# Kernel optimization log

Hardware: AMD Instinct MI355X
Metric: run time of the kernel (lower is better)

## Reference

```python
import math
import jax, jax.numpy as jnp
import numpy as np

N_HEADS = 16

def setup_inputs() -> dict:
    key = jax.random.key(0)
    k1, k2, k3 = jax.random.split(key, 3)
    B, S, D = 2, 2048, 1024
    x = jax.random.normal(k1, (B, S, D), dtype=jnp.float32)
    W_qkv = jax.random.normal(k2, (3 * D, D), dtype=jnp.float32)
    W_o = jax.random.normal(k3, (D, D), dtype=jnp.float32)
    return {"x": x, "W_qkv": W_qkv, "W_o": W_o}


def reference(x, W_qkv, W_o):
    B, S, D = x.shape
    H = N_HEADS
    d_h = D // H
    # fused QKV projection: (B,S,3D)
    t = jnp.matmul(x, W_qkv.T)
    t = t.reshape(B, S, 3, D)
    # NOTE: module reshapes (B,S,D) -> (B,H,S,d_h) directly (no transpose);
    # heads partition the flattened seq*feature layout. Replicate exactly.
    q = t[:, :, 0, :].reshape(B, H, S, d_h)
    k = t[:, :, 1, :].reshape(B, H, S, d_h)
    v = t[:, :, 2, :].reshape(B, H, S, d_h)
    # scaled by sqrt(d_model), as in the original (not sqrt(d_h))
    scores = jnp.einsum('bhqd,bhkd->bhqk', q, k) / math.sqrt(D)
    scores = jnp.tril(scores)
    # original sets ALL exact zeros to -inf (masks upper triangle)
    scores = jnp.where(scores == 0, -jnp.inf, scores)
    attn = jax.nn.softmax(scores, axis=-1)
    y_prime = jnp.matmul(attn, v)  # (B,H,S,d_h)
    y_prime = y_prime.transpose(0, 2, 1, 3).reshape(B, S, D)
    y = jnp.matmul(y_prime, W_o.T)
    return y
```

## Files before the change

### kernel.cpp

```cpp
#include <hip/hip_runtime.h>
#include <hip/hip_bf16.h>


using bf16 = __hip_bfloat16;
typedef __attribute__((ext_vector_type(8))) short bf16x8v;
typedef __attribute__((ext_vector_type(4))) float f32x4;

#define MFMA_BF16(A, B, C) __builtin_amdgcn_mfma_f32_16x16x32_bf16((A), (B), (C), 0, 0, 0)

#define GLD_LDS16(g, l)                                                        \
  __builtin_amdgcn_global_load_lds(                                            \
      (const __attribute__((address_space(1))) void*)(g),                      \
      (__attribute__((address_space(3))) void*)(l), 16, 0, 0)

static __device__ __forceinline__ unsigned short bf_bits(float f) {
  bf16 b = __float2bfloat16(f);
  return *reinterpret_cast<unsigned short*>(&b);
}

__global__ __launch_bounds__(256) void cvt_split(const float* __restrict__ in,
                                                 bf16* __restrict__ hi,
                                                 bf16* __restrict__ lo, int n) {
  int i = (blockIdx.x * 256 + threadIdx.x) * 4;
  if (i >= n) return;
  const float4 v = *(const float4*)(in + i);
  float vv[4] = {v.x, v.y, v.z, v.w};
  ushort4 hb, lb;
  unsigned short* hp = &hb.x;
  unsigned short* lp = &lb.x;
#pragma unroll
  for (int j = 0; j < 4; ++j) {
    bf16 h = __float2bfloat16(vv[j]);
    float r = vv[j] - __bfloat162float(h);
    hp[j] = bf_bits(vv[j]);
    lp[j] = bf_bits(r);
  }
  *(ushort4*)(hi + i) = hb;
  *(ushort4*)(lo + i) = lb;
}

__global__ __launch_bounds__(256) void cvt_plain(const float* __restrict__ in,
                                                 bf16* __restrict__ out, int n) {
  int i = (blockIdx.x * 256 + threadIdx.x) * 4;
  if (i >= n) return;
  const float4 v = *(const float4*)(in + i);
  ushort4 ob;
  ob.x = bf_bits(v.x); ob.y = bf_bits(v.y); ob.z = bf_bits(v.z); ob.w = bf_bits(v.w);
  *(ushort4*)(out + i) = ob;
}

__global__ __launch_bounds__(256) void gemm_qkv(
    const bf16* __restrict__ Ah, const bf16* __restrict__ Al,
    const bf16* __restrict__ Bh, const bf16* __restrict__ Bl,
    bf16* __restrict__ Qhi, bf16* __restrict__ Qlo,
    bf16* __restrict__ Khi, bf16* __restrict__ Klo,
    bf16* __restrict__ Vt) {
  const int K = 1024;
  const int NT = 24;
  __shared__ __attribute__((aligned(16))) bf16 AsH[4096], AsL[4096], BsH[4096], BsL[4096];
  const int t = threadIdx.x;
  const int lane = t & 63;
  const int wave = t >> 6;
  const int wr = wave >> 1, wc = wave & 1;
  int bid = blockIdx.x;
  bid = (bid & 7) * (768 >> 3) + (bid >> 3);
  const int bm = bid / NT, bn = bid % NT;
  const int brow = bm * 128, bcol = bn * 128;
  const bf16* pAh = Ah + (size_t)brow * K;
  const bf16* pAl = Al + (size_t)brow * K;
  const bf16* pBh = Bh + (size_t)bcol * K;
  const bf16* pBl = Bl + (size_t)bcol * K;
  const int r0 = t >> 2;
  const int c0 = (t & 3) * 8;
  f32x4 acc[4][4] = {};
  for (int k0 = 0; k0 < K; k0 += 32) {
    __syncthreads();
    GLD_LDS16(pAh + (size_t)r0 * K + k0 + c0,        &AsH[t * 8]);
    GLD_LDS16(pAh + (size_t)(r0 + 64) * K + k0 + c0, &AsH[2048 + t * 8]);
    GLD_LDS16(pAl + (size_t)r0 * K + k0 + c0,        &AsL[t * 8]);
    GLD_LDS16(pAl + (size_t)(r0 + 64) * K + k0 + c0, &AsL[2048 + t * 8]);
    GLD_LDS16(pBh + (size_t)r0 * K + k0 + c0,        &BsH[t * 8]);
    GLD_LDS16(pBh + (size_t)(r0 + 64) * K + k0 + c0, &BsH[2048 + t * 8]);
    GLD_LDS16(pBl + (size_t)r0 * K + k0 + c0,        &BsL[t * 8]);
    GLD_LDS16(pBl + (size_t)(r0 + 64) * K + k0 + c0, &BsL[2048 + t * 8]);
    __syncthreads();
    bf16x8v ah[4], al[4], bh_[4], bl_[4];
    const int ao = (wr * 64 + (lane & 15)) * 32 + (lane >> 4) * 8;
    const int bo = (wc * 64 + (lane & 15)) * 32 + (lane >> 4) * 8;
#pragma unroll
    for (int i = 0; i < 4; ++i) {
      ah[i]  = *(const bf16x8v*)&AsH[ao + i * 512];
      al[i]  = *(const bf16x8v*)&AsL[ao + i * 512];
      bh_[i] = *(const bf16x8v*)&BsH[bo + i * 512];
      bl_[i] = *(const bf16x8v*)&BsL[bo + i * 512];
    }
#pragma unroll
    for (int i = 0; i < 4; ++i)
#pragma unroll
      for (int j = 0; j < 4; ++j) {
        acc[i][j] = MFMA_BF16(ah[i], bh_[j], acc[i][j]);
        acc[i][j] = MFMA_BF16(ah[i], bl_[j], acc[i][j]);
        acc[i][j] = MFMA_BF16(al[i], bh_[j], acc[i][j]);
      }
  }
#pragma unroll
  for (int i = 0; i < 4; ++i)
#pragma unroll
    for (int j = 0; j < 4; ++j)
#pragma unroll
      for (int e = 0; e < 4; ++e) {
        const int m = brow + wr * 64 + i * 16 + ((lane >> 4) << 2) + e;
        const int n = bcol + wc * 64 + j * 16 + (lane & 15);
        float v = acc[i][j][e];
        const int b = m >> 11, s = m & 2047;
        const int c = n >> 10, d = n & 1023;
        const int bh_i = (b << 4) | (s >> 7);
        const int s2 = ((s & 127) << 4) | (d >> 6);
        const int dh = d & 63;
        if (c == 2) {
          Vt[((size_t)bh_i << 17) | ((size_t)dh << 11) | (size_t)s2] = __float2bfloat16(v);
        } else {
          if (c == 0) v *= 0.03125f;
          const size_t idx = ((size_t)bh_i << 17) | ((size_t)s2 << 6) | (size_t)dh;
          bf16 hv = __float2bfloat16(v);
          bf16 lv = __float2bfloat16(v - __bfloat162float(hv));
          if (c == 0) { Qhi[idx] = hv; Qlo[idx] = lv; }
          else        { Khi[idx] = hv; Klo[idx] = lv; }
        }
      }
}

__global__ __launch_bounds__(64) void attn_kernel(
    const bf16* __restrict__ Qhi, const bf16* __restrict__ Qlo,
    const bf16* __restrict__ Khi, const bf16* __restrict__ Klo,
    const bf16* __restrict__ Vt, bf16* __restrict__ Yp) {
  const int lane = threadIdx.x & 63;
  const int bh = blockIdx.x & 31;
  const int c  = 63 - (blockIdx.x >> 5);
  const int b = bh >> 4, h = bh & 15;
  const size_t base = (size_t)bh << 17;
  const bf16* qh_p = Qhi + base;
  const bf16* ql_p = Qlo + base;
  const bf16* kh_p = Khi + base;
  const bf16* kl_p = Klo + base;
  const bf16* v_p  = Vt + base;
  const int qbase = c << 5;
  const int l15 = lane & 15;
  const int lg  = lane >> 4;
  __shared__ __attribute__((aligned(16))) bf16 Plds[32][72];

  bf16x8v qfh[2][2], qfl[2][2];
#pragma unroll
  for (int q2 = 0; q2 < 2; ++q2)
#pragma unroll
    for (int x2 = 0; x2 < 2; ++x2) {
      const size_t o = (size_t)(qbase + q2 * 16 + l15) * 64 + x2 * 32 + lg * 8;
      qfh[q2][x2] = *(const bf16x8v*)(qh_p + o);
      qfl[q2][x2] = *(const bf16x8v*)(ql_p + o);
    }
  bf16x8v ones8;
#pragma unroll
  for (int j = 0; j < 8; ++j) ones8[j] = (short)0x3F80;

  f32x4 oac[2][4] = {};
  f32x4 oden[2] = {};
  float mrun[2] = {-3.0e38f, -3.0e38f};
  const float L2E = 1.4426950408889634f;
  const int nfull = c >> 1;

  for (int kt = 0; kt <= nfull; ++kt) {
    const int kb = kt << 6;
    f32x4 st[4][2] = {};
#pragma unroll
    for (int kf = 0; kf < 4; ++kf) {
      const size_t ko = (size_t)(kb + kf * 16 + l15) * 64 + lg * 8;
      const bf16x8v kh0 = *(const bf16x8v*)(kh_p + ko);
      const bf16x8v kh1 = *(const bf16x8v*)(kh_p + ko + 32);
      const bf16x8v kl0 = *(const bf16x8v*)(kl_p + ko);
      const bf16x8v kl1 = *(const bf16x8v*)(kl_p + ko + 32);
#pragma unroll
      for (int q2 = 0; q2 < 2; ++q2) {
        f32x4 a = st[kf][q2];
        a = MFMA_BF16(kh0, qfh[q2][0], a);
        a = MFMA_BF16(kh1, qfh[q2][1], a);
        a = MFMA_BF16(kh0, qfl[q2][0], a);
        a = MFMA_BF16(kh1, qfl[q2][1], a);
        a = MFMA_BF16(kl0, qfh[q2][0], a);
        a = MFMA_BF16(kl1, qfh[q2][1], a);
        st[kf][q2] = a;
      }
    }
    if (kt == nfull) {
#pragma unroll
      for (int kf = 0; kf < 4; ++kf)
#pragma unroll
        for (int q2 = 0; q2 < 2; ++q2)
#pragma unroll
          for (int e = 0; e < 4; ++e) {
            const int key = kb + kf * 16 + (lg << 2) + e;
            const int qr  = qbase + q2 * 16 + l15;
            if (key > qr) st[kf][q2][e] = -3.0e38f;
          }
    }
    float tmax[2] = {-3.0e38f, -3.0e38f};
#pragma unroll
    for (int kf = 0; kf < 4; ++kf)
#pragma unroll
      for (int q2 = 0; q2 < 2; ++q2)
#pragma unroll
        for (int e = 0; e < 4; ++e)
          tmax[q2] = fmaxf(tmax[q2], st[kf][q2][e]);
#pragma unroll
    for (int q2 = 0; q2 < 2; ++q2) {
      tmax[q2] = fmaxf(tmax[q2], __shfl_xor(tmax[q2], 16));
      tmax[q2] = fmaxf(tmax[q2], __shfl_xor(tmax[q2], 32));
    }
    const int ok = (tmax[0] <= mrun[0] + 8.0f) && (tmax[1] <= mrun[1] + 8.0f);
    if (!__all(ok)) {
      float sfac[2];
#pragma unroll
      for (int q2 = 0; q2 < 2; ++q2) {
        const float mn = fmaxf(mrun[q2], tmax[q2]);
        sfac[q2] = exp2f((mrun[q2] - mn) * L2E);
        mrun[q2] = mn;
      }
#pragma unroll
      for (int q2 = 0; q2 < 2; ++q2)
#pragma unroll
        for (int e = 0; e < 4; ++e) {
          const float so = __shfl(sfac[q2], (lg << 2) + e);
          oden[q2][e] *= so;
#pragma unroll
          for (int df = 0; df < 4; ++df) oac[q2][df][e] *= so;
        }
    }
    const float mL0 = mrun[0] * L2E, mL1 = mrun[1] * L2E;
#pragma unroll
    for (int kf = 0; kf < 4; ++kf)
#pragma unroll
      for (int q2 = 0; q2 < 2; ++q2) {
        const float mL = q2 ? mL1 : mL0;
        ushort4 pk;
        unsigned short* pp = &pk.x;
#pragma unroll
        for (int e = 0; e < 4; ++e) {
          const float pv = exp2f(fmaf(st[kf][q2][e], L2E, -mL));
          pp[e] = bf_bits(pv);
        }
        *(ushort4*)&Plds[q2 * 16 + l15][kf * 16 + (lg << 2)] = pk;
      }
    __syncthreads();
#pragma unroll
    for (int x2 = 0; x2 < 2; ++x2) {
      bf16x8v pa[2];
#pragma unroll
      for (int q2 = 0; q2 < 2; ++q2)
        pa[q2] = *(const bf16x8v*)&Plds[q2 * 16 + l15][x2 * 32 + lg * 8];
#pragma unroll
      for (int q2 = 0; q2 < 2; ++q2)
        oden[q2] = MFMA_BF16(pa[q2], ones8, oden[q2]);
#pragma unroll
      for (int df = 0; df < 4; ++df) {
        const bf16x8v vb =
            *(const bf16x8v*)(v_p + (size_t)(df * 16 + l15) * 2048 + kb + x2 * 32 + lg * 8);
#pragma unroll
        for (int q2 = 0; q2 < 2; ++q2)
          oac[q2][df] = MFMA_BF16(pa[q2], vb, oac[q2][df]);
      }
    }
  }
#pragma unroll
  for (int q2 = 0; q2 < 2; ++q2) {
    float li[4];
#pragma unroll
    for (int e = 0; e < 4; ++e) li[e] = 1.0f / oden[q2][e];
#pragma unroll
    for (int df = 0; df < 4; ++df)
#pragma unroll
      for (int e = 0; e < 4; ++e) {
        const int qr = qbase + q2 * 16 + (lg << 2) + e;
        const int dh = df * 16 + l15;
        Yp[(size_t)(b * 2048 + qr) * 1024 + h * 64 + dh] =
            __float2bfloat16(oac[q2][df][e] * li[e]);
      }
  }
}

__global__ __launch_bounds__(256) void gemm_out(const bf16* __restrict__ A,
                                                const bf16* __restrict__ B,
                                                float* __restrict__ C) {
  const int K = 1024;
  const int NT = 8;
  __shared__ __attribute__((aligned(16))) bf16 As[4096], Bs[4096];
  const int t = threadIdx.x;
  const int lane = t & 63;
  const int wave = t >> 6;
  const int wr = wave >> 1, wc = wave & 1;
  int bid = blockIdx.x;
  bid = (bid & 7) * (256 >> 3) + (bid >> 3);
  const int bm = bid / NT, bn = bid % NT;
  const int brow = bm * 128, bcol = bn * 128;
  const bf16* pA = A + (size_t)brow * K;
  const bf16* pB = B + (size_t)bcol * K;
  const int r0 = t >> 2;
  const int c0 = (t & 3) * 8;
  f32x4 acc[4][4] = {};
  for (int k0 = 0; k0 < K; k0 += 32) {
    __syncthreads();
    GLD_LDS16(pA + (size_t)r0 * K + k0 + c0,        &As[t * 8]);
    GLD_LDS16(pA + (size_t)(r0 + 64) * K + k0 + c0, &As[2048 + t * 8]);
    GLD_LDS16(pB + (size_t)r0 * K + k0 + c0,        &Bs[t * 8]);
    GLD_LDS16(pB + (size_t)(r0 + 64) * K + k0 + c0, &Bs[2048 + t * 8]);
    __syncthreads();
    bf16x8v af[4], bf_[4];
    const int ao = (wr * 64 + (lane & 15)) * 32 + (lane >> 4) * 8;
    const int bo = (wc * 64 + (lane & 15)) * 32 + (lane >> 4) * 8;
#pragma unroll
    for (int i = 0; i < 4; ++i) {
      af[i]  = *(const bf16x8v*)&As[ao + i * 512];
      bf_[i] = *(const bf16x8v*)&Bs[bo + i * 512];
    }
#pragma unroll
    for (int i = 0; i < 4; ++i)
#pragma unroll
      for (int j = 0; j < 4; ++j)
        acc[i][j] = MFMA_BF16(af[i], bf_[j], acc[i][j]);
  }
#pragma unroll
  for (int i = 0; i < 4; ++i)
#pragma unroll
    for (int j = 0; j < 4; ++j)
#pragma unroll
      for (int e = 0; e < 4; ++e) {
        const int m = brow + wr * 64 + i * 16 + ((lane >> 4) << 2) + e;
        const int n = bcol + wc * 64 + j * 16 + (lane & 15);
        C[(size_t)m * 1024 + n] = acc[i][j][e];
      }
}

extern "C" void kernel_launch(void* const* d_in, const int* in_sizes, int n_in,
                              void* d_out, int out_size, void* d_ws, size_t ws_size,
                              hipStream_t stream) {
  (void)in_sizes; (void)n_in; (void)out_size; (void)ws_size;
  const float* x    = (const float*)d_in[0];
  const float* wqkv = (const float*)d_in[1];
  const float* wo   = (const float*)d_in[2];
  float* out = (float*)d_out;

  const size_t NX = 4096ull * 1024;
  const size_t NW = 3072ull * 1024;
  const size_t NO = 1024ull * 1024;

  bf16* p = (bf16*)d_ws;
  bf16* xh  = p; p += NX;
  bf16* xl  = p; p += NX;
  bf16* wqh = p; p += NW;
  bf16* wql = p; p += NW;
  bf16* wob = p; p += NO;
  bf16* qhi = p; p += NX;
  bf16* qlo = p; p += NX;
  bf16* khi = p; p += NX;
  bf16* klo = p; p += NX;
  bf16* vt  = p; p += NX;
  bf16* yp  = p; p += NX;

  hipLaunchKernelGGL(cvt_split, dim3(NX / 1024), dim3(256), 0, stream, x, xh, xl, (int)NX);
  hipLaunchKernelGGL(cvt_split, dim3(NW / 1024), dim3(256), 0, stream, wqkv, wqh, wql, (int)NW);
  hipLaunchKernelGGL(cvt_plain, dim3(NO / 1024), dim3(256), 0, stream, wo, wob, (int)NO);
  hipLaunchKernelGGL(gemm_qkv, dim3(32 * 24), dim3(256), 0, stream,
                     xh, xl, wqh, wql, qhi, qlo, khi, klo, vt);
  hipLaunchKernelGGL(attn_kernel, dim3(2048), dim3(64), 0, stream,
                     qhi, qlo, khi, klo, vt, yp);
  hipLaunchKernelGGL(gemm_out, dim3(32 * 8), dim3(256), 0, stream, yp, wob, out);
}
```

Before: 337.6 us.

## Double-buffer QKV GEMM, skip lo terms for V, shrink attention and out-proj tiles

The QKV GEMM now double-buffers its LDS tiles with explicit vmcnt waits, so the next k-slice loads while the current one runs MFMAs. V-column blocks drop the lo-part loads and the two correction MFMAs, since V is stored only as a single bf16. The attention kernel goes from 32 to 16 query rows per block with twice as many blocks, and the output GEMM uses 64-row tiles with twice the grid, both to raise occupancy and balance the causal workload. In exchange, each attention block re-reads K and V for fewer queries, and the V projection loses its split-precision accuracy.

```diff
diff --git a/kernel.cpp b/kernel.cpp
--- a/kernel.cpp
+++ b/kernel.cpp
@@ -57,7 +57,8 @@
     bf16* __restrict__ Vt) {
   const int K = 1024;
   const int NT = 24;
-  __shared__ __attribute__((aligned(16))) bf16 AsH[4096], AsL[4096], BsH[4096], BsL[4096];
+  __shared__ __attribute__((aligned(16))) bf16 AsH[2][4096], AsL[2][4096],
+                                               BsH[2][4096], BsL[2][4096];
   const int t = threadIdx.x;
   const int lane = t & 63;
   const int wave = t >> 6;
@@ -66,6 +67,7 @@
   bid = (bid & 7) * (768 >> 3) + (bid >> 3);
   const int bm = bid / NT, bn = bid % NT;
   const int brow = bm * 128, bcol = bn * 128;
+  const bool isV = (bcol >= 2048);
   const bf16* pAh = Ah + (size_t)brow * K;
   const bf16* pAl = Al + (size_t)brow * K;
   const bf16* pBh = Bh + (size_t)bcol * K;
@@ -73,36 +75,71 @@
   const int r0 = t >> 2;
   const int c0 = (t & 3) * 8;
   f32x4 acc[4][4] = {};
-  for (int k0 = 0; k0 < K; k0 += 32) {
-    __syncthreads();
-    GLD_LDS16(pAh + (size_t)r0 * K + k0 + c0,        &AsH[t * 8]);
-    GLD_LDS16(pAh + (size_t)(r0 + 64) * K + k0 + c0, &AsH[2048 + t * 8]);
-    GLD_LDS16(pAl + (size_t)r0 * K + k0 + c0,        &AsL[t * 8]);
-    GLD_LDS16(pAl + (size_t)(r0 + 64) * K + k0 + c0, &AsL[2048 + t * 8]);
-    GLD_LDS16(pBh + (size_t)r0 * K + k0 + c0,        &BsH[t * 8]);
-    GLD_LDS16(pBh + (size_t)(r0 + 64) * K + k0 + c0, &BsH[2048 + t * 8]);
-    GLD_LDS16(pBl + (size_t)r0 * K + k0 + c0,        &BsL[t * 8]);
-    GLD_LDS16(pBl + (size_t)(r0 + 64) * K + k0 + c0, &BsL[2048 + t * 8]);
-    __syncthreads();
-    bf16x8v ah[4], al[4], bh_[4], bl_[4];
-    const int ao = (wr * 64 + (lane & 15)) * 32 + (lane >> 4) * 8;
-    const int bo = (wc * 64 + (lane & 15)) * 32 + (lane >> 4) * 8;
+
+#define STAGE(buf, k0_)                                                        \
+  {                                                                            \
+    const int _k = (k0_);                                                      \
+    GLD_LDS16(pAh + (size_t)r0 * K + _k + c0,        &AsH[buf][t * 8]);        \
+    GLD_LDS16(pAh + (size_t)(r0 + 64) * K + _k + c0, &AsH[buf][2048 + t * 8]); \
+    GLD_LDS16(pBh + (size_t)r0 * K + _k + c0,        &BsH[buf][t * 8]);        \
+    GLD_LDS16(pBh + (size_t)(r0 + 64) * K + _k + c0, &BsH[buf][2048 + t * 8]); \
+    if (!isV) {                                                                \
+      GLD_LDS16(pAl + (size_t)r0 * K + _k + c0,        &AsL[buf][t * 8]);      \
+      GLD_LDS16(pAl + (size_t)(r0 + 64) * K + _k + c0, &AsL[buf][2048 + t * 8]);\
+      GLD_LDS16(pBl + (size_t)r0 * K + _k + c0,        &BsL[buf][t * 8]);      \
+      GLD_LDS16(pBl + (size_t)(r0 + 64) * K + _k + c0, &BsL[buf][2048 + t * 8]);\
+    }                                                                          \
+  }
+
+  STAGE(0, 0);
+  const int ao = (wr * 64 + (lane & 15)) * 32 + (lane >> 4) * 8;
+  const int bo = (wc * 64 + (lane & 15)) * 32 + (lane >> 4) * 8;
+  for (int tk = 0; tk < 32; ++tk) {
+    const int cur = tk & 1;
+    if (tk < 31) {
+      STAGE(cur ^ 1, (tk + 1) * 32);
+      if (!isV) asm volatile("s_waitcnt vmcnt(8)" ::: "memory");
+      else      asm volatile("s_waitcnt vmcnt(4)" ::: "memory");
+    } else {
+      asm volatile("s_waitcnt vmcnt(0)" ::: "memory");
+    }
+    __builtin_amdgcn_sched_barrier(0);
+    __builtin_amdgcn_s_barrier();
+    asm volatile("" ::: "memory");
+    bf16x8v ah[4], bh_[4];
 #pragma unroll
     for (int i = 0; i < 4; ++i) {
-      ah[i]  = *(const bf16x8v*)&AsH[ao + i * 512];
-      al[i]  = *(const bf16x8v*)&AsL[ao + i * 512];
-      bh_[i] = *(const bf16x8v*)&BsH[bo + i * 512];
-      bl_[i] = *(const bf16x8v*)&BsL[bo + i * 512];
-    }
-#pragma unroll
-    for (int i = 0; i < 4; ++i)
-#pragma unroll
-      for (int j = 0; j < 4; ++j) {
-        acc[i][j] = MFMA_BF16(ah[i], bh_[j], acc[i][j]);
-        acc[i][j] = MFMA_BF16(ah[i], bl_[j], acc[i][j]);
-        acc[i][j] = MFMA_BF16(al[i], bh_[j], acc[i][j]);
-      }
-  }
+      ah[i]  = *(const bf16x8v*)&AsH[cur][ao + i * 512];
+      bh_[i] = *(const bf16x8v*)&BsH[cur][bo + i * 512];
+    }
+    if (!isV) {
+      bf16x8v al[4], bl_[4];
+#pragma unroll
+      for (int i = 0; i < 4; ++i) {
+        al[i]  = *(const bf16x8v*)&AsL[cur][ao + i * 512];
+        bl_[i] = *(const bf16x8v*)&BsL[cur][bo + i * 512];
+      }
+#pragma unroll
+      for (int i = 0; i < 4; ++i)
+#pragma unroll
+        for (int j = 0; j < 4; ++j) {
+          acc[i][j] = MFMA_BF16(ah[i], bh_[j], acc[i][j]);
+          acc[i][j] = MFMA_BF16(ah[i], bl_[j], acc[i][j]);
+          acc[i][j] = MFMA_BF16(al[i], bh_[j], acc[i][j]);
+        }
+    } else {
+#pragma unroll
+      for (int i = 0; i < 4; ++i)
+#pragma unroll
+        for (int j = 0; j < 4; ++j)
+          acc[i][j] = MFMA_BF16(ah[i], bh_[j], acc[i][j]);
+    }
+    asm volatile("" ::: "memory");
+    __builtin_amdgcn_sched_barrier(0);
+    __builtin_amdgcn_s_barrier();
+    asm volatile("" ::: "memory");
+  }
+#undef STAGE
 #pragma unroll
   for (int i = 0; i < 4; ++i)
 #pragma unroll
@@ -130,13 +167,13 @@
       }
 }
 
-__global__ __launch_bounds__(64) void attn_kernel(
+__global__ __launch_bounds__(64, 4) void attn_kernel(
     const bf16* __restrict__ Qhi, const bf16* __restrict__ Qlo,
     const bf16* __restrict__ Khi, const bf16* __restrict__ Klo,
     const bf16* __restrict__ Vt, bf16* __restrict__ Yp) {
   const int lane = threadIdx.x & 63;
   const int bh = blockIdx.x & 31;
-  const int c  = 63 - (blockIdx.x >> 5);
+  const int c  = 127 - (blockIdx.x >> 5);
   const int b = bh >> 4, h = bh & 15;
   const size_t base = (size_t)bh << 17;
   const bf16* qh_p = Qhi + base;
@@ -144,33 +181,31 @@
   const bf16* kh_p = Khi + base;
   const bf16* kl_p = Klo + base;
   const bf16* v_p  = Vt + base;
-  const int qbase = c << 5;
+  const int qbase = c << 4;
   const int l15 = lane & 15;
   const int lg  = lane >> 4;
-  __shared__ __attribute__((aligned(16))) bf16 Plds[32][72];
-
-  bf16x8v qfh[2][2], qfl[2][2];
-#pragma unroll
-  for (int q2 = 0; q2 < 2; ++q2)
-#pragma unroll
-    for (int x2 = 0; x2 < 2; ++x2) {
-      const size_t o = (size_t)(qbase + q2 * 16 + l15) * 64 + x2 * 32 + lg * 8;
-      qfh[q2][x2] = *(const bf16x8v*)(qh_p + o);
-      qfl[q2][x2] = *(const bf16x8v*)(ql_p + o);
-    }
+  __shared__ __attribute__((aligned(16))) bf16 Plds[16][72];
+
+  bf16x8v qfh[2], qfl[2];
+#pragma unroll
+  for (int x2 = 0; x2 < 2; ++x2) {
+    const size_t o = (size_t)(qbase + l15) * 64 + x2 * 32 + lg * 8;
+    qfh[x2] = *(const bf16x8v*)(qh_p + o);
+    qfl[x2] = *(const bf16x8v*)(ql_p + o);
+  }
   bf16x8v ones8;
 #pragma unroll
   for (int j = 0; j < 8; ++j) ones8[j] = (short)0x3F80;
 
-  f32x4 oac[2][4] = {};
-  f32x4 oden[2] = {};
-  float mrun[2] = {-3.0e38f, -3.0e38f};
+  f32x4 oac[4] = {};
+  f32x4 oden = {};
+  float mrun = -3.0e38f;
   const float L2E = 1.4426950408889634f;
-  const int nfull = c >> 1;
+  const int nfull = c >> 2;
 
   for (int kt = 0; kt <= nfull; ++kt) {
     const int kb = kt << 6;
-    f32x4 st[4][2] = {};
+    f32x4 st[4] = {};
 #pragma unroll
     for (int kf = 0; kf < 4; ++kf) {
       const size_t ko = (size_t)(kb + kf * 16 + l15) * 64 + lg * 8;
@@ -178,112 +213,84 @@
       const bf16x8v kh1 = *(const bf16x8v*)(kh_p + ko + 32);
       const bf16x8v kl0 = *(const bf16x8v*)(kl_p + ko);
       const bf16x8v kl1 = *(const bf16x8v*)(kl_p + ko + 32);
-#pragma unroll
-      for (int q2 = 0; q2 < 2; ++q2) {
-        f32x4 a = st[kf][q2];
-        a = MFMA_BF16(kh0, qfh[q2][0], a);
-        a = MFMA_BF16(kh1, qfh[q2][1], a);
-        a = MFMA_BF16(kh0, qfl[q2][0], a);
-        a = MFMA_BF16(kh1, qfl[q2][1], a);
-        a = MFMA_BF16(kl0, qfh[q2][0], a);
-        a = MFMA_BF16(kl1, qfh[q2][1], a);
-        st[kf][q2] = a;
-      }
+      f32x4 a = st[kf];
+      a = MFMA_BF16(kh0, qfh[0], a);
+      a = MFMA_BF16(kh1, qfh[1], a);
+      a = MFMA_BF16(kh0, qfl[0], a);
+      a = MFMA_BF16(kh1, qfl[1], a);
+      a = MFMA_BF16(kl0, qfh[0], a);
+      a = MFMA_BF16(kl1, qfh[1], a);
+      st[kf] = a;
     }
     if (kt == nfull) {
 #pragma unroll
       for (int kf = 0; kf < 4; ++kf)
 #pragma unroll
-        for (int q2 = 0; q2 < 2; ++q2)
-#pragma unroll
-          for (int e = 0; e < 4; ++e) {
-            const int key = kb + kf * 16 + (lg << 2) + e;
-            const int qr  = qbase + q2 * 16 + l15;
-            if (key > qr) st[kf][q2][e] = -3.0e38f;
-          }
-    }
-    float tmax[2] = {-3.0e38f, -3.0e38f};
+        for (int e = 0; e < 4; ++e) {
+          const int key = kb + kf * 16 + (lg << 2) + e;
+          const int qr  = qbase + l15;
+          if (key > qr) st[kf][e] = -3.0e38f;
+        }
+    }
+    float tmax = -3.0e38f;
 #pragma unroll
     for (int kf = 0; kf < 4; ++kf)
 #pragma unroll
-      for (int q2 = 0; q2 < 2; ++q2)
-#pragma unroll
-        for (int e = 0; e < 4; ++e)
-          tmax[q2] = fmaxf(tmax[q2], st[kf][q2][e]);
-#pragma unroll
-    for (int q2 = 0; q2 < 2; ++q2) {
-      tmax[q2] = fmaxf(tmax[q2], __shfl_xor(tmax[q2], 16));
-      tmax[q2] = fmaxf(tmax[q2], __shfl_xor(tmax[q2], 32));
-    }
-    const int ok = (tmax[0] <= mrun[0] + 8.0f) && (tmax[1] <= mrun[1] + 8.0f);
-    if (!__all(ok)) {
-      float sfac[2];
-#pragma unroll
-      for (int q2 = 0; q2 < 2; ++q2) {
-        const float mn = fmaxf(mrun[q2], tmax[q2]);
-        sfac[q2] = exp2f((mrun[q2] - mn) * L2E);
-        mrun[q2] = mn;
-      }
-#pragma unroll
-      for (int q2 = 0; q2 < 2; ++q2)
-#pragma unroll
-        for (int e = 0; e < 4; ++e) {
-          const float so = __shfl(sfac[q2], (lg << 2) + e);
-          oden[q2][e] *= so;
-#pragma unroll
-          for (int df = 0; df < 4; ++df) oac[q2][df][e] *= so;
-        }
-    }
-    const float mL0 = mrun[0] * L2E, mL1 = mrun[1] * L2E;
-#pragma unroll
-    for (int kf = 0; kf < 4; ++kf)
-#pragma unroll
-      for (int q2 = 0; q2 < 2; ++q2) {
-        const float mL = q2 ? mL1 : mL0;
-        ushort4 pk;
-        unsigned short* pp = &pk.x;
-#pragma unroll
-        for (int e = 0; e < 4; ++e) {
-          const float pv = exp2f(fmaf(st[kf][q2][e], L2E, -mL));
-          pp[e] = bf_bits(pv);
-        }
-        *(ushort4*)&Plds[q2 * 16 + l15][kf * 16 + (lg << 2)] = pk;
-      }
-    __syncthreads();
+      for (int e = 0; e < 4; ++e) tmax = fmaxf(tmax, st[kf][e]);
+    tmax = fmaxf(tmax, __shfl_xor(tmax, 16));
+    tmax = fmaxf(tmax, __shfl_xor(tmax, 32));
+    if (!__all(tmax <= mrun + 8.0f)) {
+      const float mn = fmaxf(mrun, tmax);
+      const float sfac = exp2f((mrun - mn) * L2E);
+      mrun = mn;
+#pragma unroll
+      for (int e = 0; e < 4; ++e) {
+        const float so = __shfl(sfac, (lg << 2) + e);
+        oden[e] *= so;
+#pragma unroll
+        for (int df = 0; df < 4; ++df) oac[df][e] *= so;
+      }
+    }
+    const float mL = mrun * L2E;
+#pragma unroll
+    for (int kf = 0; kf < 4; ++kf) {
+      ushort4 pk;
+      unsigned short* pp = &pk.x;
+#pragma unroll
+      for (int e = 0; e < 4; ++e)
+        pp[e] = bf_bits(exp2f(fmaf(st[kf][e], L2E, -mL)));
+      *(ushort4*)&Plds[l15][kf * 16 + (lg << 2)] = pk;
+    }
+    asm volatile("s_waitcnt lgkmcnt(0)" ::: "memory");
+    __builtin_amdgcn_sched_barrier(0);
+    bf16x8v pa[2];
+#pragma unroll
+    for (int x2 = 0; x2 < 2; ++x2)
+      pa[x2] = *(const bf16x8v*)&Plds[l15][x2 * 32 + lg * 8];
+    asm volatile("" ::: "memory");
 #pragma unroll
     for (int x2 = 0; x2 < 2; ++x2) {
-      bf16x8v pa[2];
-#pragma unroll
-      for (int q2 = 0; q2 < 2; ++q2)
-        pa[q2] = *(const bf16x8v*)&Plds[q2 * 16 + l15][x2 * 32 + lg * 8];
-#pragma unroll
-      for (int q2 = 0; q2 < 2; ++q2)
-        oden[q2] = MFMA_BF16(pa[q2], ones8, oden[q2]);
+      oden = MFMA_BF16(pa[x2], ones8, oden);
 #pragma unroll
       for (int df = 0; df < 4; ++df) {
         const bf16x8v vb =
             *(const bf16x8v*)(v_p + (size_t)(df * 16 + l15) * 2048 + kb + x2 * 32 + lg * 8);
-#pragma unroll
-        for (int q2 = 0; q2 < 2; ++q2)
-          oac[q2][df] = MFMA_BF16(pa[q2], vb, oac[q2][df]);
-      }
-    }
-  }
-#pragma unroll
-  for (int q2 = 0; q2 < 2; ++q2) {
-    float li[4];
-#pragma unroll
-    for (int e = 0; e < 4; ++e) li[e] = 1.0f / oden[q2][e];
-#pragma unroll
-    for (int df = 0; df < 4; ++df)
-#pragma unroll
-      for (int e = 0; e < 4; ++e) {
-        const int qr = qbase + q2 * 16 + (lg << 2) + e;
-        const int dh = df * 16 + l15;
-        Yp[(size_t)(b * 2048 + qr) * 1024 + h * 64 + dh] =
-            __float2bfloat16(oac[q2][df][e] * li[e]);
-      }
-  }
+        oac[df] = MFMA_BF16(pa[x2], vb, oac[df]);
+      }
+    }
+  }
+  float li[4];
+#pragma unroll
+  for (int e = 0; e < 4; ++e) li[e] = 1.0f / oden[e];
+#pragma unroll
+  for (int df = 0; df < 4; ++df)
+#pragma unroll
+    for (int e = 0; e < 4; ++e) {
+      const int qr = qbase + (lg << 2) + e;
+      const int dh = df * 16 + l15;
+      Yp[(size_t)(b * 2048 + qr) * 1024 + h * 64 + dh] =
+          __float2bfloat16(oac[df][e] * li[e]);
+    }
 }
 
 __global__ __launch_bounds__(256) void gemm_out(const bf16* __restrict__ A,
@@ -291,48 +298,49 @@
                                                 float* __restrict__ C) {
   const int K = 1024;
   const int NT = 8;
-  __shared__ __attribute__((aligned(16))) bf16 As[4096], Bs[4096];
+  __shared__ __attribute__((aligned(16))) bf16 As[2048], Bs[4096];
   const int t = threadIdx.x;
   const int lane = t & 63;
   const int wave = t >> 6;
   const int wr = wave >> 1, wc = wave & 1;
   int bid = blockIdx.x;
-  bid = (bid & 7) * (256 >> 3) + (bid >> 3);
+  bid = (bid & 7) * (512 >> 3) + (bid >> 3);
   const int bm = bid / NT, bn = bid % NT;
-  const int brow = bm * 128, bcol = bn * 128;
+  const int brow = bm * 64, bcol = bn * 128;
   const bf16* pA = A + (size_t)brow * K;
   const bf16* pB = B + (size_t)bcol * K;
   const int r0 = t >> 2;
   const int c0 = (t & 3) * 8;
-  f32x4 acc[4][4] = {};
+  f32x4 acc[2][4] = {};
   for (int k0 = 0; k0 < K; k0 += 32) {
     __syncthreads();
     GLD_LDS16(pA + (size_t)r0 * K + k0 + c0,        &As[t * 8]);
-    GLD_LDS16(pA + (size_t)(r0 + 64) * K + k0 + c0, &As[2048 + t * 8]);
     GLD_LDS16(pB + (size_t)r0 * K + k0 + c0,        &Bs[t * 8]);
     GLD_LDS16(pB + (size_t)(r0 + 64) * K + k0 + c0, &Bs[2048 + t * 8]);
     __syncthreads();
-    bf16x8v af[4], bf_[4];
-    const int ao = (wr * 64 + (lane & 15)) * 32 + (lane >> 4) * 8;
-    const int bo = (wc * 64 + (lane & 15)) * 32 + (lane >> 4) * 8;
-#pragma unroll
-    for (int i = 0; i < 4; ++i) {
-      af[i]  = *(const bf16x8v*)&As[ao + i * 512];
-      bf_[i] = *(const bf16x8v*)&Bs[bo + i * 512];
-    }
-#pragma unroll
-    for (int i = 0; i < 4; ++i)
+    bf16x8v af[2], bf_[4];
+    const int l15 = lane & 15, lg = lane >> 4;
+#pragma unroll
+    for (int i = 0; i < 2; ++i)
+      af[i] = *(const bf16x8v*)&As[(wr * 32 + i * 16 + l15) * 32 + lg * 8];
+#pragma unroll
+    for (int j = 0; j < 4; ++j) {
+      const int rB = wc * 64 + j * 16 + l15;
+      bf_[j] = *(const bf16x8v*)&Bs[(rB & 63) * 32 + (rB >> 6) * 2048 + lg * 8];
+    }
+#pragma unroll
+    for (int i = 0; i < 2; ++i)
 #pragma unroll
       for (int j = 0; j < 4; ++j)
         acc[i][j] = MFMA_BF16(af[i], bf_[j], acc[i][j]);
   }
 #pragma unroll
-  for (int i = 0; i < 4; ++i)
+  for (int i = 0; i < 2; ++i)
 #pragma unroll
     for (int j = 0; j < 4; ++j)
 #pragma unroll
       for (int e = 0; e < 4; ++e) {
-        const int m = brow + wr * 64 + i * 16 + ((lane >> 4) << 2) + e;
+        const int m = brow + wr * 32 + i * 16 + ((lane >> 4) << 2) + e;
         const int n = bcol + wc * 64 + j * 16 + (lane & 15);
         C[(size_t)m * 1024 + n] = acc[i][j][e];
       }
@@ -369,7 +377,7 @@
   hipLaunchKernelGGL(cvt_plain, dim3(NO / 1024), dim3(256), 0, stream, wo, wob, (int)NO);
   hipLaunchKernelGGL(gemm_qkv, dim3(32 * 24), dim3(256), 0, stream,
                      xh, xl, wqh, wql, qhi, qlo, khi, klo, vt);
-  hipLaunchKernelGGL(attn_kernel, dim3(2048), dim3(64), 0, stream,
+  hipLaunchKernelGGL(attn_kernel, dim3(4096), dim3(64), 0, stream,
                      qhi, qlo, khi, klo, vt, yp);
-  hipLaunchKernelGGL(gemm_out, dim3(32 * 8), dim3(256), 0, stream, yp, wob, out);
-}
+  hipLaunchKernelGGL(gemm_out, dim3(64 * 8), dim3(256), 0, stream, yp, wob, out);
+}
```

New measurement: 397.6 us. +17.8%, slower.
